# Optimization experiments

Hardware: AMD Instinct MI355X
Metric: run time of the kernel (lower is better)

## Reference

```python
import jax, jax.numpy as jnp
import numpy as np

D_MODEL = 512
NUM_HEADS = 8


def setup_inputs() -> dict:
    key = jax.random.key(0)
    ks = jax.random.split(key, 12)
    B, S, D = 2, 4096, D_MODEL
    s = 1.0 / np.sqrt(D)
    return {
        "q": jax.random.normal(ks[0], (B, S, D), jnp.float32),
        "k": jax.random.normal(ks[1], (B, S, D), jnp.float32),
        "v": jax.random.normal(ks[2], (B, S, D), jnp.float32),
        "w_q": jax.random.normal(ks[3], (D, D), jnp.float32) * s,
        "b_q": jax.random.normal(ks[4], (D,), jnp.float32) * s,
        "w_k": jax.random.normal(ks[5], (D, D), jnp.float32) * s,
        "b_k": jax.random.normal(ks[6], (D,), jnp.float32) * s,
        "w_v": jax.random.normal(ks[7], (D, D), jnp.float32) * s,
        "b_v": jax.random.normal(ks[8], (D,), jnp.float32) * s,
        "w_o": jax.random.normal(ks[9], (D, D), jnp.float32) * s,
        "b_o": jax.random.normal(ks[10], (D,), jnp.float32) * s,
    }


def _split(x, num_heads):
    B, S, D = x.shape
    return x.reshape(B, S, num_heads, D // num_heads).transpose(0, 2, 1, 3)


def reference(q, k, v, w_q, b_q, w_k, b_k, w_v, b_v, w_o, b_o):
    # Linear projections (torch Linear: x @ W^T + b)
    qp = q @ w_q.T + b_q
    kp = k @ w_k.T + b_k
    vp = v @ w_v.T + b_v
    # split into heads: [B, H, S, d_head]
    qh = _split(qp, NUM_HEADS)
    kh = _split(kp, NUM_HEADS)
    vh = _split(vp, NUM_HEADS)
    d_head = qh.shape[-1]
    # NOTE: original scales by sqrt(d_model of the per-head tensor) == sqrt(d_head)
    score = jnp.einsum("bhqd,bhkd->bhqk", qh, kh) / jnp.sqrt(jnp.float32(d_head))
    attn = jax.nn.softmax(score, axis=-1)  # full [B,H,S,S] materialized, as in source
    out = jnp.einsum("bhqk,bhkd->bhqd", attn, vh)
    # concat heads back to [B, S, D]
    B, H, S, Dh = out.shape
    out = out.transpose(0, 2, 1, 3).reshape(B, S, H * Dh)
    return out @ w_o.T + b_o
```

## Files before the change

kernel.cpp:

```cpp
#include <hip/hip_runtime.h>
#include <math.h>

typedef __bf16 bf16_t;
typedef __bf16 bf16x4_v __attribute__((ext_vector_type(4)));
typedef __bf16 bf16x8_t __attribute__((ext_vector_type(8)));
typedef float f32x4_t __attribute__((ext_vector_type(4)));
typedef unsigned uint2_t __attribute__((ext_vector_type(2)));
typedef unsigned uint4_t __attribute__((ext_vector_type(4)));

#define S_LEN 4096
#define DM 512
#define NH 8
#define DH 64
#define MTOT 8192

#define Q_SCALE 0.1803368801111204f

#define REG   4194304
#define WREG  262144
#define W_OFF (3 * REG)
#define CVT_TOTAL (3 * REG + 4 * WREG)
#define QH_OFF CVT_TOTAL

__device__ inline f32x4_t mfma16(bf16x8_t a, bf16x8_t b, f32x4_t c) {
    return __builtin_amdgcn_mfma_f32_16x16x32_bf16(a, b, c, 0, 0, 0);
}

__device__ inline unsigned pkbf16(float a, float b) {
    unsigned short ra = __builtin_bit_cast(unsigned short, (bf16_t)a);
    unsigned short rb = __builtin_bit_cast(unsigned short, (bf16_t)b);
    return (unsigned)ra | ((unsigned)rb << 16);
}

__device__ inline void async_copy16(const void* g, void* l) {
    __builtin_amdgcn_global_load_lds(
        (const __attribute__((address_space(1))) void*)g,
        (__attribute__((address_space(3))) void*)l, 16, 0, 0);
}

__global__ __launch_bounds__(256) void cvt_all(
    const float* __restrict__ q, const float* __restrict__ k, const float* __restrict__ v,
    const float* __restrict__ wq, const float* __restrict__ wk,
    const float* __restrict__ wv, const float* __restrict__ wo,
    bf16_t* __restrict__ dst)
{
    long gidx = (long)blockIdx.x * 2048 + (long)threadIdx.x * 8;
    const float* src;
    long off = gidx;
    if      (gidx < 1L * REG)          { src = q; }
    else if (gidx < 2L * REG)          { src = k;  off = gidx - 1L * REG; }
    else if (gidx < 3L * REG)          { src = v;  off = gidx - 2L * REG; }
    else if (gidx < W_OFF + 1L * WREG) { src = wq; off = gidx - W_OFF; }
    else if (gidx < W_OFF + 2L * WREG) { src = wk; off = gidx - (W_OFF + 1L * WREG); }
    else if (gidx < W_OFF + 3L * WREG) { src = wv; off = gidx - (W_OFF + 2L * WREG); }
    else                               { src = wo; off = gidx - (W_OFF + 3L * WREG); }
    float4 a = *(const float4*)(src + off);
    float4 b = *(const float4*)(src + off + 4);
    bf16x8_t h;
    h[0] = (bf16_t)a.x; h[1] = (bf16_t)a.y; h[2] = (bf16_t)a.z; h[3] = (bf16_t)a.w;
    h[4] = (bf16_t)b.x; h[5] = (bf16_t)b.y; h[6] = (bf16_t)b.z; h[7] = (bf16_t)b.w;
    *(bf16x8_t*)(dst + gidx) = h;
}

__global__ __launch_bounds__(256) void gemm_qkv(
    const bf16_t* __restrict__ XWb,
    const float* __restrict__ B0, const float* __restrict__ B1, const float* __restrict__ B2,
    bf16_t* __restrict__ dst_base)
{
    const int p = blockIdx.z;
    const bf16_t* __restrict__ X = XWb + (size_t)p * REG;
    const bf16_t* __restrict__ W = XWb + W_OFF + (size_t)p * WREG;
    const float* __restrict__ Bi = (p == 0) ? B0 : ((p == 1) ? B1 : B2);
    bf16_t* __restrict__ dst = dst_base + (size_t)p * REG;

    const int m0 = blockIdx.x * 128;
    const int n0 = blockIdx.y * 128;
    const int tid = threadIdx.x;
    const int lane = tid & 63, wid = tid >> 6;
    const int lm = lane & 15, lg = lane >> 4;
    const int wm = (wid >> 1) * 64, wn = (wid & 1) * 64;

    __shared__ __align__(16) char gsmem[65536];

    f32x4_t acc[4][4] = {};

    const int r0 = tid >> 3, c7 = tid & 7;
    const int cA0 = ((lg) ^ (lm & 7)) * 8;
    const int cA1 = ((4 + lg) ^ (lm & 7)) * 8;

#pragma unroll
    for (int i = 0; i < 4; ++i) {
        int row = i * 32 + r0;
        int ch = c7 ^ (row & 7);
        async_copy16(X + (size_t)(m0 + row) * DM + ch * 8, gsmem + (i * 256 + tid) * 16);
        async_copy16(W + (size_t)(n0 + row) * DM + ch * 8, gsmem + 16384 + (i * 256 + tid) * 16);
    }

    for (int kb = 0; kb < DM / 64; ++kb) {
        __syncthreads();
        if (kb + 1 < DM / 64) {
            const int k0 = (kb + 1) * 64;
            char* nb = gsmem + ((kb + 1) & 1) * 32768;
#pragma unroll
            for (int i = 0; i < 4; ++i) {
                int row = i * 32 + r0;
                int ch = c7 ^ (row & 7);
                async_copy16(X + (size_t)(m0 + row) * DM + k0 + ch * 8, nb + (i * 256 + tid) * 16);
                async_copy16(W + (size_t)(n0 + row) * DM + k0 + ch * 8, nb + 16384 + (i * 256 + tid) * 16);
            }
        }
        const bf16_t* As = (const bf16_t*)(gsmem + (kb & 1) * 32768);
        const bf16_t* Bs = (const bf16_t*)(gsmem + (kb & 1) * 32768 + 16384);
#pragma unroll
        for (int kd = 0; kd < 2; ++kd) {
            const int co = kd ? cA1 : cA0;
            bf16x8_t fa[4], fb[4];
#pragma unroll
            for (int mt = 0; mt < 4; ++mt) {
                fa[mt] = *(const bf16x8_t*)(As + (wm + mt * 16 + lm) * 64 + co);
                fb[mt] = *(const bf16x8_t*)(Bs + (wn + mt * 16 + lm) * 64 + co);
            }
            if (p < 2) {
#pragma unroll
                for (int mt = 0; mt < 4; ++mt)
#pragma unroll
                    for (int nt = 0; nt < 4; ++nt)
                        acc[nt][mt] = mfma16(fb[nt], fa[mt], acc[nt][mt]);
            } else {
#pragma unroll
                for (int mt = 0; mt < 4; ++mt)
#pragma unroll
                    for (int nt = 0; nt < 4; ++nt)
                        acc[mt][nt] = mfma16(fa[mt], fb[nt], acc[mt][nt]);
            }
        }
    }

    if (p == 2) {
        __syncthreads();
        bf16_t* tb = (bf16_t*)gsmem;
#pragma unroll
        for (int nt = 0; nt < 4; ++nt) {
            int colL = wn + nt * 16 + lm;
            float bv = Bi[n0 + colL];
#pragma unroll
            for (int mt = 0; mt < 4; ++mt) {
                int sL = wm + mt * 16 + lg * 4;
                bf16x4_v pk;
#pragma unroll
                for (int r = 0; r < 4; ++r) pk[r] = (bf16_t)(acc[mt][nt][r] + bv);
                int byte = colL * 256 + ((((sL >> 3) ^ (colL & 15))) * 16) + (sL & 7) * 2;
                *(bf16x4_v*)((char*)tb + byte) = pk;
            }
        }
        __syncthreads();
        {
            const int colL = tid >> 1, half = tid & 1;
            const int col = n0 + colL;
            const int h = (col >> 6) & 7, dc = col & 63;
            const int bb = m0 >> 12, s0 = m0 & (S_LEN - 1);
            size_t base = (((size_t)(bb * NH + h)) * DH + dc) * S_LEN + s0;
#pragma unroll
            for (int j = 0; j < 8; ++j) {
                int chunk = half * 8 + j;
                bf16x8_t v = *(const bf16x8_t*)((char*)tb + colL * 256 + ((chunk ^ (colL & 15)) * 16));
                *(bf16x8_t*)&dst[base + chunk * 8] = v;
            }
        }
    } else {
        const float scale = (p == 0) ? Q_SCALE : 1.0f;
#pragma unroll
        for (int nt = 0; nt < 4; ++nt) {
            int ncol = n0 + wn + nt * 16 + lg * 4;
            float4 bv4 = *(const float4*)&Bi[ncol];
            int h = (ncol >> 6) & 7, dc = ncol & 63;
#pragma unroll
            for (int mt = 0; mt < 4; ++mt) {
                int m = m0 + wm + mt * 16 + lm;
                int bb = m >> 12, s = m & (S_LEN - 1);
                bf16x4_v pk;
                pk[0] = (bf16_t)((acc[nt][mt][0] + bv4.x) * scale);
                pk[1] = (bf16_t)((acc[nt][mt][1] + bv4.y) * scale);
                pk[2] = (bf16_t)((acc[nt][mt][2] + bv4.z) * scale);
                pk[3] = (bf16_t)((acc[nt][mt][3] + bv4.w) * scale);
                *(bf16x4_v*)&dst[(((size_t)(bb * NH + h)) * S_LEN + s) * DH + dc] = pk;
            }
        }
    }
}

__global__ __launch_bounds__(256, 2) void flash_attn(
    const bf16_t* __restrict__ Qh, const bf16_t* __restrict__ Kh,
    const bf16_t* __restrict__ Vth, bf16_t* __restrict__ O)
{
    const int bh = blockIdx.y;
    const int q0 = blockIdx.x * 128;
    const int tid = threadIdx.x;
    const int lane = tid & 63, wid = tid >> 6;
    const int lm = lane & 15, lg = lane >> 4;
    const int qg = wid & 1;
    const int kvh = wid >> 1;

    const bf16_t* __restrict__ Qb  = Qh  + (size_t)bh * S_LEN * DH;
    const bf16_t* __restrict__ Kb  = Kh  + (size_t)bh * S_LEN * DH;
    const bf16_t* __restrict__ Vtg = Vth + (size_t)bh * S_LEN * DH;

    __shared__ __align__(16) char smem[65536];

    bf16x8_t bQ[4][2];
#pragma unroll
    for (int nt = 0; nt < 4; ++nt)
#pragma unroll
        for (int kd = 0; kd < 2; ++kd)
            bQ[nt][kd] = *(const bf16x8_t*)(Qb + (size_t)(q0 + qg * 64 + nt * 16 + lm) * DH + kd * 32 + lg * 8);

    f32x4_t o_acc[4][4] = {};
    f32x4_t l4[4] = {};

    const uint4_t onesu = {0x3F803F80u, 0x3F803F80u, 0x3F803F80u, 0x3F803F80u};
    const bf16x8_t vOnes = __builtin_bit_cast(bf16x8_t, onesu);

    const int srow = tid >> 3;
    const int slch = (tid & 7) ^ (srow & 7);
    const bf16_t* gK = Kb + (size_t)srow * DH + slch * 8;
    const bf16_t* gV = Vtg + (size_t)srow * S_LEN + slch * 8;

    const int cK0 = ((lg) ^ (lm & 7)) * 16;
    const int cK1 = ((4 + lg) ^ (lm & 7)) * 16;

    {
        char* b = smem;
#pragma unroll
        for (int i = 0; i < 4; ++i)
            async_copy16(gK + (size_t)(32 * i) * DH, b + i * 4096 + tid * 16);
#pragma unroll
        for (int i = 0; i < 4; ++i)
            async_copy16(gV + (size_t)(i & 1) * 32 * S_LEN + (i >> 1) * 64,
                         b + 16384 + i * 4096 + tid * 16);
    }

    const int NT = S_LEN / 128;
    for (int it = 0; it < NT; ++it) {
        const char* buf = smem + (it & 1) * 32768;
        __syncthreads();

        if (it + 1 < NT) {
            char* nb = smem + ((it + 1) & 1) * 32768;
            const int kvb = (it + 1) * 128;
#pragma unroll
            for (int i = 0; i < 4; ++i)
                async_copy16(gK + (size_t)(kvb + 32 * i) * DH, nb + i * 4096 + tid * 16);
#pragma unroll
            for (int i = 0; i < 4; ++i)
                async_copy16(gV + (size_t)(i & 1) * 32 * S_LEN + kvb + (i >> 1) * 64,
                             nb + 16384 + i * 4096 + tid * 16);
        }

        const char* ksb = buf + kvh * 8192;
        const char* vsb = buf + 16384 + kvh * 8192;

        uint4_t pq[2][4];
#pragma unroll
        for (int mt = 0; mt < 4; ++mt) {
            const char* krow = ksb + (mt * 16 + lm) * 128;
            bf16x8_t aK0 = *(const bf16x8_t*)(krow + cK0);
            bf16x8_t aK1 = *(const bf16x8_t*)(krow + cK1);
            const int cc = mt >> 1, hf = (mt & 1) * 2;
#pragma unroll
            for (int nt = 0; nt < 4; ++nt) {
                f32x4_t s = {};
                s = mfma16(aK0, bQ[nt][0], s);
                s = mfma16(aK1, bQ[nt][1], s);
                float e0 = __builtin_amdgcn_exp2f(s[0]);
                float e1 = __builtin_amdgcn_exp2f(s[1]);
                float e2 = __builtin_amdgcn_exp2f(s[2]);
                float e3 = __builtin_amdgcn_exp2f(s[3]);
                pq[cc][nt][hf + 0] = pkbf16(e0, e1);
                pq[cc][nt][hf + 1] = pkbf16(e2, e3);
            }
        }

#pragma unroll
        for (int cc = 0; cc < 2; ++cc)
#pragma unroll
            for (int nt = 0; nt < 4; ++nt)
                l4[nt] = mfma16(vOnes, __builtin_bit_cast(bf16x8_t, pq[cc][nt]), l4[nt]);

#pragma unroll
        for (int mt = 0; mt < 4; ++mt) {
            const char* vrow = vsb + (mt * 16 + lm) * 128;
#pragma unroll
            for (int cc = 0; cc < 2; ++cc) {
                const int ca = 2 * cc, cb = 2 * cc + 1;
                int pc0 = (ca * 2 + (lg >> 1)) ^ (lm & 7);
                int pc1 = (cb * 2 + (lg >> 1)) ^ (lm & 7);
                uint2_t va0 = *(const uint2_t*)(vrow + pc0 * 16 + (lg & 1) * 8);
                uint2_t va1 = *(const uint2_t*)(vrow + pc1 * 16 + (lg & 1) * 8);
                bf16x8_t vA = __builtin_bit_cast(bf16x8_t, (uint4_t){va0[0], va0[1], va1[0], va1[1]});
#pragma unroll
                for (int nt = 0; nt < 4; ++nt)
                    o_acc[mt][nt] = mfma16(vA, __builtin_bit_cast(bf16x8_t, pq[cc][nt]), o_acc[mt][nt]);
            }
        }
    }

    __syncthreads();

    float* ob = (float*)smem + qg * (64 * 68);
    float* lb = (float*)(smem + 34816);

    if (kvh == 1) {
#pragma unroll
        for (int nt = 0; nt < 4; ++nt) {
#pragma unroll
            for (int mt = 0; mt < 4; ++mt)
                *(f32x4_t*)&ob[(nt * 16 + lm) * 68 + mt * 16 + lg * 4] = o_acc[mt][nt];
            if (lg == 0) lb[qg * 64 + nt * 16 + lm] = l4[nt][0];
        }
    }
    __syncthreads();
    if (kvh == 0) {
        const int bb = bh >> 3, h = bh & 7;
#pragma unroll
        for (int nt = 0; nt < 4; ++nt) {
            float ltot = l4[nt][0] + lb[qg * 64 + nt * 16 + lm];
            float inv = 1.0f / ltot;
            int q = q0 + qg * 64 + nt * 16 + lm;
            size_t base = ((size_t)(bb * S_LEN + q)) * DM + h * DH;
#pragma unroll
            for (int mt = 0; mt < 4; ++mt) {
                f32x4_t orow = *(const f32x4_t*)&ob[(nt * 16 + lm) * 68 + mt * 16 + lg * 4];
                bf16x4_v pkd;
#pragma unroll
                for (int r = 0; r < 4; ++r)
                    pkd[r] = (bf16_t)((o_acc[mt][nt][r] + orow[r]) * inv);
                *(bf16x4_v*)&O[base + mt * 16 + lg * 4] = pkd;
            }
        }
    }
}

__global__ __launch_bounds__(256) void gemm_out(
    const bf16_t* __restrict__ A, const bf16_t* __restrict__ W,
    const float* __restrict__ Bi, float* __restrict__ out)
{
    const int m0 = blockIdx.x * 64;
    const int n0 = blockIdx.y * 128;
    const int tid = threadIdx.x;
    const int lane = tid & 63, wid = tid >> 6;
    const int lm = lane & 15, lg = lane >> 4;
    const int wm = (wid >> 1) * 32, wn = (wid & 1) * 64;

    __shared__ __align__(16) char gsmem[49152];

    f32x4_t acc[4][2] = {};

    const int r0 = tid >> 3, c7 = tid & 7;
    const int cA0 = ((lg) ^ (lm & 7)) * 8;
    const int cA1 = ((4 + lg) ^ (lm & 7)) * 8;

#pragma unroll
    for (int i = 0; i < 2; ++i) {
        int idx = i * 256 + tid;
        int row = idx >> 3;
        int ch = (idx & 7) ^ (row & 7);
        async_copy16(A + (size_t)(m0 + row) * DM + ch * 8, gsmem + idx * 16);
    }
#pragma unroll
    for (int i = 0; i < 4; ++i) {
        int row = i * 32 + r0;
        int ch = c7 ^ (row & 7);
        async_copy16(W + (size_t)(n0 + row) * DM + ch * 8, gsmem + 8192 + (i * 256 + tid) * 16);
    }

    for (int kb = 0; kb < DM / 64; ++kb) {
        __syncthreads();
        if (kb + 1 < DM / 64) {
            const int k0 = (kb + 1) * 64;
            char* nb = gsmem + ((kb + 1) & 1) * 24576;
#pragma unroll
            for (int i = 0; i < 2; ++i) {
                int idx = i * 256 + tid;
                int row = idx >> 3;
                int ch = (idx & 7) ^ (row & 7);
                async_copy16(A + (size_t)(m0 + row) * DM + k0 + ch * 8, nb + idx * 16);
            }
#pragma unroll
            for (int i = 0; i < 4; ++i) {
                int row = i * 32 + r0;
                int ch = c7 ^ (row & 7);
                async_copy16(W + (size_t)(n0 + row) * DM + k0 + ch * 8, nb + 8192 + (i * 256 + tid) * 16);
            }
        }
        const bf16_t* As = (const bf16_t*)(gsmem + (kb & 1) * 24576);
        const bf16_t* Bs = (const bf16_t*)(gsmem + (kb & 1) * 24576 + 8192);
#pragma unroll
        for (int kd = 0; kd < 2; ++kd) {
            const int co = kd ? cA1 : cA0;
            bf16x8_t fa[2], fb[4];
#pragma unroll
            for (int mt = 0; mt < 2; ++mt)
                fa[mt] = *(const bf16x8_t*)(As + (wm + mt * 16 + lm) * 64 + co);
#pragma unroll
            for (int nt = 0; nt < 4; ++nt)
                fb[nt] = *(const bf16x8_t*)(Bs + (wn + nt * 16 + lm) * 64 + co);
#pragma unroll
            for (int nt = 0; nt < 4; ++nt)
#pragma unroll
                for (int mt = 0; mt < 2; ++mt)
                    acc[nt][mt] = mfma16(fb[nt], fa[mt], acc[nt][mt]);
        }
    }

#pragma unroll
    for (int nt = 0; nt < 4; ++nt) {
        int ncol = n0 + wn + nt * 16 + lg * 4;
        float4 bv4 = *(const float4*)&Bi[ncol];
#pragma unroll
        for (int mt = 0; mt < 2; ++mt) {
            int m = m0 + wm + mt * 16 + lm;
            float4 ov;
            ov.x = acc[nt][mt][0] + bv4.x;
            ov.y = acc[nt][mt][1] + bv4.y;
            ov.z = acc[nt][mt][2] + bv4.z;
            ov.w = acc[nt][mt][3] + bv4.w;
            *(float4*)&out[(size_t)m * DM + ncol] = ov;
        }
    }
}

extern "C" void kernel_launch(void* const* d_in, const int* in_sizes, int n_in,
                              void* d_out, int out_size, void* d_ws, size_t ws_size,
                              hipStream_t stream)
{
    const float* q  = (const float*)d_in[0];
    const float* k  = (const float*)d_in[1];
    const float* v  = (const float*)d_in[2];
    const float* wq = (const float*)d_in[3];
    const float* bq = (const float*)d_in[4];
    const float* wk = (const float*)d_in[5];
    const float* bk = (const float*)d_in[6];
    const float* wv = (const float*)d_in[7];
    const float* bv = (const float*)d_in[8];
    const float* wo = (const float*)d_in[9];
    const float* bo = (const float*)d_in[10];
    float* out = (float*)d_out;

    bf16_t* ws = (bf16_t*)d_ws;
    bf16_t* XWb = ws;
    bf16_t* Qh  = ws + QH_OFF;
    bf16_t* Kh  = Qh + REG;
    bf16_t* VTh = Kh + REG;
    bf16_t* Ob  = ws;
    bf16_t* Wob = ws + W_OFF + 3 * (size_t)WREG;

    cvt_all<<<CVT_TOTAL / 2048, 256, 0, stream>>>(q, k, v, wq, wk, wv, wo, XWb);

    dim3 g1(MTOT / 128, DM / 128, 3);
    gemm_qkv<<<g1, 256, 0, stream>>>(XWb, bq, bk, bv, Qh);

    dim3 g2(S_LEN / 128, 2 * NH, 1);
    flash_attn<<<g2, 256, 0, stream>>>(Qh, Kh, VTh, Ob);

    dim3 g3(MTOT / 64, DM / 128, 1);
    gemm_out<<<g3, 256, 0, stream>>>(Ob, Wob, bo, out);
}
```

Baseline: 216.7 us.

## Fuse fp32-to-bf16 activation conversion into QKV GEMM loads

Stops converting q/k/v activations to bf16 in a separate pass. The QKV GEMM now loads fp32 activations into registers, prefetching the next k-block, and converts them to bf16 before writing to shared memory after the MFMA work. The conversion kernel only handles the weights, and the workspace layout is rearranged so the attention output no longer aliases the converted activations. This removes a full read/write round trip of the activations, but each GEMM block now reads twice the bytes and uses more registers for the prefetch.

```diff
diff --git a/kernel.cpp b/kernel.cpp
--- a/kernel.cpp
+++ b/kernel.cpp
@@ -18,9 +18,7 @@
 
 #define REG   4194304
 #define WREG  262144
-#define W_OFF (3 * REG)
-#define CVT_TOTAL (3 * REG + 4 * WREG)
-#define QH_OFF CVT_TOTAL
+#define QH_OFF (4 * WREG)
 
 __device__ inline f32x4_t mfma16(bf16x8_t a, bf16x8_t b, f32x4_t c) {
     return __builtin_amdgcn_mfma_f32_16x16x32_bf16(a, b, c, 0, 0, 0);
@@ -38,38 +36,36 @@
         (__attribute__((address_space(3))) void*)l, 16, 0, 0);
 }
 
-__global__ __launch_bounds__(256) void cvt_all(
-    const float* __restrict__ q, const float* __restrict__ k, const float* __restrict__ v,
+__device__ inline bf16x8_t cvt8(float4 a, float4 b) {
+    bf16x8_t h;
+    h[0] = (bf16_t)a.x; h[1] = (bf16_t)a.y; h[2] = (bf16_t)a.z; h[3] = (bf16_t)a.w;
+    h[4] = (bf16_t)b.x; h[5] = (bf16_t)b.y; h[6] = (bf16_t)b.z; h[7] = (bf16_t)b.w;
+    return h;
+}
+
+__global__ __launch_bounds__(256) void cvt_w(
     const float* __restrict__ wq, const float* __restrict__ wk,
     const float* __restrict__ wv, const float* __restrict__ wo,
     bf16_t* __restrict__ dst)
 {
     long gidx = (long)blockIdx.x * 2048 + (long)threadIdx.x * 8;
-    const float* src;
-    long off = gidx;
-    if      (gidx < 1L * REG)          { src = q; }
-    else if (gidx < 2L * REG)          { src = k;  off = gidx - 1L * REG; }
-    else if (gidx < 3L * REG)          { src = v;  off = gidx - 2L * REG; }
-    else if (gidx < W_OFF + 1L * WREG) { src = wq; off = gidx - W_OFF; }
-    else if (gidx < W_OFF + 2L * WREG) { src = wk; off = gidx - (W_OFF + 1L * WREG); }
-    else if (gidx < W_OFF + 3L * WREG) { src = wv; off = gidx - (W_OFF + 2L * WREG); }
-    else                               { src = wo; off = gidx - (W_OFF + 3L * WREG); }
+    int p = (int)(gidx >> 18);
+    long off = gidx & (WREG - 1);
+    const float* src = (p == 0) ? wq : ((p == 1) ? wk : ((p == 2) ? wv : wo));
     float4 a = *(const float4*)(src + off);
     float4 b = *(const float4*)(src + off + 4);
-    bf16x8_t h;
-    h[0] = (bf16_t)a.x; h[1] = (bf16_t)a.y; h[2] = (bf16_t)a.z; h[3] = (bf16_t)a.w;
-    h[4] = (bf16_t)b.x; h[5] = (bf16_t)b.y; h[6] = (bf16_t)b.z; h[7] = (bf16_t)b.w;
-    *(bf16x8_t*)(dst + gidx) = h;
+    *(bf16x8_t*)(dst + gidx) = cvt8(a, b);
 }
 
 __global__ __launch_bounds__(256) void gemm_qkv(
-    const bf16_t* __restrict__ XWb,
+    const float* __restrict__ Xq, const float* __restrict__ Xk, const float* __restrict__ Xv,
+    const bf16_t* __restrict__ Wb,
     const float* __restrict__ B0, const float* __restrict__ B1, const float* __restrict__ B2,
     bf16_t* __restrict__ dst_base)
 {
     const int p = blockIdx.z;
-    const bf16_t* __restrict__ X = XWb + (size_t)p * REG;
-    const bf16_t* __restrict__ W = XWb + W_OFF + (size_t)p * WREG;
+    const float* __restrict__ X = (p == 0) ? Xq : ((p == 1) ? Xk : Xv);
+    const bf16_t* __restrict__ W = Wb + (size_t)p * WREG;
     const float* __restrict__ Bi = (p == 0) ? B0 : ((p == 1) ? B1 : B2);
     bf16_t* __restrict__ dst = dst_base + (size_t)p * REG;
 
@@ -88,25 +84,36 @@
     const int cA0 = ((lg) ^ (lm & 7)) * 8;
     const int cA1 = ((4 + lg) ^ (lm & 7)) * 8;
 
-#pragma unroll
-    for (int i = 0; i < 4; ++i) {
-        int row = i * 32 + r0;
-        int ch = c7 ^ (row & 7);
-        async_copy16(X + (size_t)(m0 + row) * DM + ch * 8, gsmem + (i * 256 + tid) * 16);
-        async_copy16(W + (size_t)(n0 + row) * DM + ch * 8, gsmem + 16384 + (i * 256 + tid) * 16);
+    {
+        float4 xa[4], xb[4];
+#pragma unroll
+        for (int i = 0; i < 4; ++i) {
+            int row = i * 32 + r0;
+            int ch = c7 ^ (row & 7);
+            const float* sx = X + (size_t)(m0 + row) * DM + ch * 8;
+            xa[i] = *(const float4*)sx;
+            xb[i] = *(const float4*)(sx + 4);
+            async_copy16(W + (size_t)(n0 + row) * DM + ch * 8, gsmem + 16384 + (i * 256 + tid) * 16);
+        }
+#pragma unroll
+        for (int i = 0; i < 4; ++i)
+            *(bf16x8_t*)(gsmem + (i * 256 + tid) * 16) = cvt8(xa[i], xb[i]);
     }
 
     for (int kb = 0; kb < DM / 64; ++kb) {
         __syncthreads();
+        float4 pa[4], pb[4];
+        char* nb = gsmem + ((kb + 1) & 1) * 32768;
         if (kb + 1 < DM / 64) {
-            const int k0 = (kb + 1) * 64;
-            char* nb = gsmem + ((kb + 1) & 1) * 32768;
+            const int k0n = (kb + 1) * 64;
 #pragma unroll
             for (int i = 0; i < 4; ++i) {
                 int row = i * 32 + r0;
                 int ch = c7 ^ (row & 7);
-                async_copy16(X + (size_t)(m0 + row) * DM + k0 + ch * 8, nb + (i * 256 + tid) * 16);
-                async_copy16(W + (size_t)(n0 + row) * DM + k0 + ch * 8, nb + 16384 + (i * 256 + tid) * 16);
+                const float* sx = X + (size_t)(m0 + row) * DM + k0n + ch * 8;
+                pa[i] = *(const float4*)sx;
+                pb[i] = *(const float4*)(sx + 4);
+                async_copy16(W + (size_t)(n0 + row) * DM + k0n + ch * 8, nb + 16384 + (i * 256 + tid) * 16);
             }
         }
         const bf16_t* As = (const bf16_t*)(gsmem + (kb & 1) * 32768);
@@ -133,6 +140,11 @@
                     for (int nt = 0; nt < 4; ++nt)
                         acc[mt][nt] = mfma16(fa[mt], fb[nt], acc[mt][nt]);
             }
+        }
+        if (kb + 1 < DM / 64) {
+#pragma unroll
+            for (int i = 0; i < 4; ++i)
+                *(bf16x8_t*)(nb + (i * 256 + tid) * 16) = cvt8(pa[i], pb[i]);
         }
     }
 
@@ -447,17 +459,17 @@
     float* out = (float*)d_out;
 
     bf16_t* ws = (bf16_t*)d_ws;
-    bf16_t* XWb = ws;
+    bf16_t* Wb  = ws;
     bf16_t* Qh  = ws + QH_OFF;
     bf16_t* Kh  = Qh + REG;
     bf16_t* VTh = Kh + REG;
-    bf16_t* Ob  = ws;
-    bf16_t* Wob = ws + W_OFF + 3 * (size_t)WREG;
-
-    cvt_all<<<CVT_TOTAL / 2048, 256, 0, stream>>>(q, k, v, wq, wk, wv, wo, XWb);
+    bf16_t* Ob  = VTh + REG;
+    bf16_t* Wob = ws + 3 * (size_t)WREG;
+
+    cvt_w<<<(4 * WREG) / 2048, 256, 0, stream>>>(wq, wk, wv, wo, Wb);
 
     dim3 g1(MTOT / 128, DM / 128, 3);
-    gemm_qkv<<<g1, 256, 0, stream>>>(XWb, bq, bk, bv, Qh);
+    gemm_qkv<<<g1, 256, 0, stream>>>(q, k, v, Wb, bq, bk, bv, Qh);
 
     dim3 g2(S_LEN / 128, 2 * NH, 1);
     flash_attn<<<g2, 256, 0, stream>>>(Qh, Kh, VTh, Ob);
```

New measurement: 220.4 us. Within noise of the previous version (+1.7%).
